# Kernel tuning notes

Hardware: AMD Instinct MI355X
Metric: run time of the kernel (lower is better)

Reference implementation:

```python
import jax, jax.numpy as jnp
import numpy as np

N_NODES = 100000
N_EDGES = 1280000
N_REL = 8
DIM = 64
N_LAYERS = 2
N_TGT = 50000


def setup_inputs() -> dict:
    key = jax.random.key(0)
    ks = jax.random.split(key, 8)
    x_idx = jnp.arange(N_NODES, dtype=jnp.int64) if jax.config.jax_enable_x64 else jnp.arange(N_NODES, dtype=jnp.int32)
    edge_index = jax.random.randint(ks[0], (2, N_EDGES), 0, N_NODES)
    edge_type = jax.random.randint(ks[1], (N_EDGES,), 0, N_REL)
    target_edge_index = jax.random.randint(ks[2], (2, N_TGT), 0, N_NODES)
    # xavier-ish scales to keep activations stable through relu stack
    node_emb = jax.random.normal(ks[3], (N_NODES, DIM), dtype=jnp.float32) * 0.1
    weight = jax.random.normal(ks[4], (N_LAYERS, N_REL, DIM, DIM), dtype=jnp.float32) * (1.0 / np.sqrt(DIM))
    root = jax.random.normal(ks[5], (N_LAYERS, DIM, DIM), dtype=jnp.float32) * (1.0 / np.sqrt(DIM))
    bias = jax.random.normal(ks[6], (N_LAYERS, DIM), dtype=jnp.float32) * 0.01
    return {"x_idx": x_idx, "edge_index": edge_index, "edge_type": edge_type,
            "target_edge_index": target_edge_index, "node_emb": node_emb,
            "weight": weight, "root": root, "bias": bias}


def reference(x_idx, edge_index, edge_type, target_edge_index, node_emb, weight, root, bias):
    # RGCN forward: x = node_emb[x_idx]; L x (FastRGCNConv + relu); edge dot-product score.
    x = node_emb[x_idx]                       # [N, D]
    src, dst = edge_index[0], edge_index[1]   # messages flow src -> dst (PyG source_to_target)
    n = x.shape[0]
    # in-degree for 'mean' aggregation (zero-degree nodes get 0, guard div)
    deg = jax.ops.segment_sum(jnp.ones((src.shape[0],), dtype=x.dtype), dst, num_segments=n)
    inv_deg = (1.0 / jnp.maximum(deg, 1.0))[:, None]  # [N, 1]
    n_layers = weight.shape[0]
    for l in range(n_layers):
        # transform every node by every relation, then gather per edge (FastRGCNConv math)
        h = jnp.einsum('ni,rio->rno', x, weight[l])   # [R, N, D]
        msg = h[edge_type, src]                       # [E, D]
        agg = jax.ops.segment_sum(msg, dst, num_segments=n) * inv_deg  # mean aggr [N, D]
        x = jax.nn.relu(agg + x @ root[l] + bias[l])
    s, t = target_edge_index[0], target_edge_index[1]
    return jnp.sum(x[s] * x[t], axis=-1)              # [T]
```

## Files before the change

### kernel.cpp

```cpp
#include <hip/hip_runtime.h>
#include <hip/hip_bf16.h>

#define DIM 64
#define NREL 8
#define KTOT 576

typedef __bf16 bf16x8 __attribute__((ext_vector_type(8)));
typedef __bf16 bf16x4 __attribute__((ext_vector_type(4)));
typedef float  f32x4  __attribute__((ext_vector_type(4)));

__global__ __launch_bounds__(256) void histgather_kernel(const int* __restrict__ dst,
                                                         const int* __restrict__ et,
                                                         int* __restrict__ deg8,
                                                         int* __restrict__ eoff,
                                                         const int* __restrict__ x_idx,
                                                         const float* __restrict__ emb,
                                                         __bf16* __restrict__ xb0,
                                                         __bf16* __restrict__ hbuf,
                                                         int* __restrict__ srcs,
                                                         int N, int E, int epad_cap) {
    int i = blockIdx.x * 256 + threadIdx.x;
    if (i < N * DIM) {
        int n = i >> 6;
        int c = i & 63;
        xb0[i] = (__bf16)emb[(size_t)x_idx[n] * DIM + c];
    }
    if (i < DIM) {
        hbuf[(size_t)N * NREL * DIM + i] = (__bf16)0.f;
    }
    if (i < epad_cap) srcs[i] = N * NREL;
    if (i < E) eoff[i] = atomicAdd(&deg8[dst[i] * 8 + et[i]], 1);
}

__global__ __launch_bounds__(256) void scan1_kernel(const int* __restrict__ deg8,
                                                    int* __restrict__ offs,
                                                    int* __restrict__ bsum,
                                                    float* __restrict__ invdeg, int N) {
    __shared__ int sd[256];
    int tid = threadIdx.x;
    int d = blockIdx.x * 256 + tid;
    int vpad = 0;
    if (d < N) {
        int vtrue = 0;
#pragma unroll
        for (int r = 0; r < NREL; ++r) vtrue += deg8[d * 8 + r];
        vpad = (vtrue + 3) & ~3;
        invdeg[d] = 1.0f / fmaxf((float)vtrue, 1.0f);
    }
    sd[tid] = vpad;
    __syncthreads();
#pragma unroll
    for (int off = 1; off < 256; off <<= 1) {
        int t = (tid >= off) ? sd[tid - off] : 0;
        __syncthreads();
        sd[tid] += t;
        __syncthreads();
    }
    if (d < N) offs[d] = sd[tid] - vpad;
    if (tid == 255) bsum[blockIdx.x] = sd[255];
}

__global__ __launch_bounds__(512) void scan2wcat_kernel(int* __restrict__ bsum, int nb,
                                                        const float* __restrict__ weight,
                                                        const float* __restrict__ root,
                                                        __bf16* __restrict__ Wt2, int L) {
    if (blockIdx.x == 0) {
        __shared__ int sd[512];
        int tid = threadIdx.x;
        int v = (tid < nb) ? bsum[tid] : 0;
        sd[tid] = v;
        __syncthreads();
#pragma unroll
        for (int off = 1; off < 512; off <<= 1) {
            int t = (tid >= off) ? sd[tid - off] : 0;
            __syncthreads();
            sd[tid] += t;
            __syncthreads();
        }
        if (tid < nb) bsum[tid] = sd[tid] - v;
    } else {
        int idx = (blockIdx.x - 1) * 512 + threadIdx.x;
        int total = L * KTOT * DIM;
        if (idx >= total) return;
        int l = idx / (KTOT * DIM);
        int rem = idx - l * (KTOT * DIM);
        int row = rem / DIM;
        int ch = rem - row * DIM;
        float w;
        if (row < 512) {
            int r = row >> 6, c = row & 63;
            w = weight[(((l * 8 + r) * 64) + ch) * 64 + c];
        } else {
            w = root[(l * 64 + ch) * 64 + (row - 512)];
        }
        Wt2[idx] = (__bf16)w;
    }
}

__global__ __launch_bounds__(256) void rpbuild_kernel(const int* __restrict__ deg8,
                                                      const int* __restrict__ offs,
                                                      const int* __restrict__ bsum,
                                                      int* __restrict__ rp,
                                                      int N) {
    int d = blockIdx.x * 256 + threadIdx.x;
    if (d >= N) return;
    int base = offs[d] + bsum[blockIdx.x];
    int run = 0;
#pragma unroll
    for (int r = 0; r < NREL; ++r) {
        rp[d * 8 + r] = base + run;
        run += deg8[d * 8 + r];
    }
    if (d == N - 1) rp[(size_t)N * 8] = base + ((run + 3) & ~3);
}

__global__ __launch_bounds__(256) void bucket_kernel(const int* __restrict__ src,
                                                     const int* __restrict__ dst,
                                                     const int* __restrict__ et,
                                                     const int* __restrict__ rp,
                                                     const int* __restrict__ eoff,
                                                     int* __restrict__ srcs, int E) {
    int i = blockIdx.x * 256 + threadIdx.x;
    int half = (E + 1) >> 1;
    if (i >= half) return;
    int iB = i + half;
    bool hasB = iB < E;
    int etA = et[i];
    int etB = hasB ? et[iB] : 0;
    int cellA = dst[i] * 8 + etA;
    int cellB = hasB ? dst[iB] * 8 + etB : 0;
    int rA = rp[cellA];
    int rB = hasB ? rp[cellB] : 0;
    int oA = eoff[i];
    int oB = hasB ? eoff[iB] : 0;
    int sA = src[i];
    int sB = hasB ? src[iB] : 0;
    srcs[rA + oA] = sA * NREL + etA;
    if (hasB) srcs[rB + oB] = sB * NREL + etB;
}

__global__ __launch_bounds__(256) void transform_kernel(const __bf16* __restrict__ xin,
                                                        const __bf16* __restrict__ Wt2,
                                                        __bf16* __restrict__ h, int N) {
    int wave = threadIdx.x >> 6;
    int lane = threadIdx.x & 63;
    int l15 = lane & 15;
    int lg  = lane >> 4;

    bf16x8 afrag[8][2];
#pragma unroll
    for (int p = 0; p < 8; ++p) {
        const __bf16* wrow = Wt2 + (size_t)(p * 64 + 16 * wave + l15) * DIM + lg * 8;
        afrag[p][0] = *reinterpret_cast<const bf16x8*>(wrow);
        afrag[p][1] = *reinterpret_cast<const bf16x8*>(wrow + 32);
    }
    int cb = 16 * wave + 4 * lg;

    int ntiles = (N + 15) >> 4;
    for (int tile = blockIdx.x; tile < ntiles; tile += gridDim.x) {
        int n = tile * 16 + l15;
        int nc = (n < N) ? n : (N - 1);
        const __bf16* xrow = xin + (size_t)nc * DIM + lg * 8;
        bf16x8 bv0 = *reinterpret_cast<const bf16x8*>(xrow);
        bf16x8 bv1 = *reinterpret_cast<const bf16x8*>(xrow + 32);

#pragma unroll
        for (int p = 0; p < 8; ++p) {
            f32x4 acc = (f32x4){0.f, 0.f, 0.f, 0.f};
            acc = __builtin_amdgcn_mfma_f32_16x16x32_bf16(afrag[p][0], bv0, acc, 0, 0, 0);
            acc = __builtin_amdgcn_mfma_f32_16x16x32_bf16(afrag[p][1], bv1, acc, 0, 0, 0);
            if (n < N) {
                bf16x4 hv;
#pragma unroll
                for (int i = 0; i < 4; ++i) hv[i] = (__bf16)acc[i];
                *reinterpret_cast<bf16x4*>(h + (size_t)n * (NREL * DIM) + p * 64 + cb) = hv;
            }
        }
    }
}

__global__ __launch_bounds__(256) void aggroot_kernel(const __bf16* __restrict__ h,
                                                      const __bf16* __restrict__ xin,
                                                      const int* __restrict__ srcs,
                                                      const int* __restrict__ rp,
                                                      const float* __restrict__ invdeg,
                                                      const __bf16* __restrict__ Wt2,
                                                      const float* __restrict__ bias_l,
                                                      __bf16* __restrict__ xout, int N) {
    __shared__ __align__(16) float S16[16][68];
    int wave = threadIdx.x >> 6;
    int lane = threadIdx.x & 63;
    int l15 = lane & 15;
    int lg  = lane >> 4;

    bf16x8 ar0, ar1;
    {
        const __bf16* wrow = Wt2 + (size_t)(512 + 16 * wave + l15) * DIM + lg * 8;
        ar0 = *reinterpret_cast<const bf16x8*>(wrow);
        ar1 = *reinterpret_cast<const bf16x8*>(wrow + 32);
    }
    int cbase = 16 * wave + 4 * lg;
    f32x4 bias4 = *reinterpret_cast<const f32x4*>(bias_l + cbase);

    int tile = blockIdx.x;

#pragma unroll
    for (int rr = 0; rr < 4; ++rr) {
        int d0 = tile * 16 + wave * 4 + rr;
        if (d0 >= N) d0 = N - 1;
        int d = __builtin_amdgcn_readfirstlane(d0);
        int qb = rp[d * 8];
        int qe = rp[d * 8 + 8];
        float acc = 0.f;
        int q = qb;
        for (; q + 8 <= qe; q += 8) {
            int4 sa = *reinterpret_cast<const int4*>(srcs + q);
            int4 sb = *reinterpret_cast<const int4*>(srcs + q + 4);
            float v0 = (float)h[(size_t)sa.x * DIM + lane];
            float v1 = (float)h[(size_t)sa.y * DIM + lane];
            float v2 = (float)h[(size_t)sa.z * DIM + lane];
            float v3 = (float)h[(size_t)sa.w * DIM + lane];
            float v4 = (float)h[(size_t)sb.x * DIM + lane];
            float v5 = (float)h[(size_t)sb.y * DIM + lane];
            float v6 = (float)h[(size_t)sb.z * DIM + lane];
            float v7 = (float)h[(size_t)sb.w * DIM + lane];
            acc += ((v0 + v1) + (v2 + v3)) + ((v4 + v5) + (v6 + v7));
        }
        if (q < qe) {
            int4 sa = *reinterpret_cast<const int4*>(srcs + q);
            float v0 = (float)h[(size_t)sa.x * DIM + lane];
            float v1 = (float)h[(size_t)sa.y * DIM + lane];
            float v2 = (float)h[(size_t)sa.z * DIM + lane];
            float v3 = (float)h[(size_t)sa.w * DIM + lane];
            acc += (v0 + v1) + (v2 + v3);
        }
        S16[wave * 4 + rr][lane] = acc * invdeg[d];
    }
    __syncthreads();

    int n = tile * 16 + l15;
    int nc = (n < N) ? n : (N - 1);
    const __bf16* xrow = xin + (size_t)nc * DIM + lg * 8;
    bf16x8 bv0 = *reinterpret_cast<const bf16x8*>(xrow);
    bf16x8 bv1 = *reinterpret_cast<const bf16x8*>(xrow + 32);
    f32x4 acc = (f32x4){0.f, 0.f, 0.f, 0.f};
    acc = __builtin_amdgcn_mfma_f32_16x16x32_bf16(ar0, bv0, acc, 0, 0, 0);
    acc = __builtin_amdgcn_mfma_f32_16x16x32_bf16(ar1, bv1, acc, 0, 0, 0);

    if (n < N) {
        f32x4 ag = *reinterpret_cast<const f32x4*>(&S16[l15][cbase]);
        bf16x4 hv;
#pragma unroll
        for (int i = 0; i < 4; ++i)
            hv[i] = (__bf16)fmaxf(acc[i] + ag[i] + bias4[i], 0.f);
        *reinterpret_cast<bf16x4*>(xout + (size_t)n * DIM + cbase) = hv;
    }
}

__global__ __launch_bounds__(256) void score_kernel(const __bf16* __restrict__ xb,
                                                    const int* __restrict__ s,
                                                    const int* __restrict__ t,
                                                    float* __restrict__ out, int T) {
    int i = blockIdx.x * 4 + (threadIdx.x >> 6);
    if (i >= T) return;
    int lane = threadIdx.x & 63;
    float p = (float)xb[(size_t)s[i] * DIM + lane] * (float)xb[(size_t)t[i] * DIM + lane];
#pragma unroll
    for (int off = 32; off > 0; off >>= 1) p += __shfl_down(p, off, 64);
    if (lane == 0) out[i] = p;
}

extern "C" void kernel_launch(void* const* d_in, const int* in_sizes, int n_in,
                              void* d_out, int out_size, void* d_ws, size_t ws_size,
                              hipStream_t stream) {
    const int*   x_idx  = (const int*)d_in[0];
    const int*   eidx   = (const int*)d_in[1];
    const int*   etyp   = (const int*)d_in[2];
    const int*   tidx   = (const int*)d_in[3];
    const float* emb    = (const float*)d_in[4];
    const float* weight = (const float*)d_in[5];
    const float* root   = (const float*)d_in[6];
    const float* bias   = (const float*)d_in[7];

    int N = in_sizes[0];
    int E = in_sizes[2];
    int T = in_sizes[3] / 2;
    int L = in_sizes[5] / (NREL * DIM * DIM);

    const int* src = eidx;
    const int* dst = eidx + E;
    const int* ts  = tidx;
    const int* tt  = tidx + T;
    float* out = (float*)d_out;

    int epad_cap = E + 3 * N + 64;

    char* p = (char*)d_ws;
    auto alloc = [&](size_t bytes) -> void* {
        void* r = (void*)p;
        p += (bytes + 255) & ~(size_t)255;
        return r;
    };
    __bf16* hbuf    = (__bf16*)alloc(((size_t)N * NREL + 1) * DIM * sizeof(__bf16));
    __bf16* xb0     = (__bf16*)alloc((size_t)N * DIM * sizeof(__bf16));
    __bf16* xb1     = (__bf16*)alloc((size_t)N * DIM * sizeof(__bf16));
    __bf16* Wt2     = (__bf16*)alloc((size_t)L * KTOT * DIM * sizeof(__bf16));
    int*    srcs    = (int*)   alloc((size_t)epad_cap * sizeof(int));
    int*    eoff    = (int*)   alloc((size_t)E * sizeof(int));
    int*    deg8    = (int*)   alloc((size_t)N * 8 * sizeof(int));
    int*    rp      = (int*)   alloc(((size_t)N * 8 + 1) * sizeof(int));
    int*    offs    = (int*)   alloc((size_t)N * sizeof(int));
    float*  invdeg  = (float*) alloc((size_t)N * sizeof(float));
    int*    bsum    = (int*)   alloc(1024 * sizeof(int));

    int nb = (N + 255) / 256;
    int ntiles = (N + 15) / 16;

    hipMemsetAsync(deg8, 0, (size_t)N * 8 * sizeof(int), stream);
    histgather_kernel<<<((size_t)N * DIM + 255) / 256, 256, 0, stream>>>(
        dst, etyp, deg8, eoff, x_idx, emb, xb0, hbuf, srcs, N, E, epad_cap);
    scan1_kernel<<<nb, 256, 0, stream>>>(deg8, offs, bsum, invdeg, N);
    {
        int wtotal = L * KTOT * DIM;
        int wblocks = 1 + (wtotal + 511) / 512;
        scan2wcat_kernel<<<wblocks, 512, 0, stream>>>(bsum, nb, weight, root, Wt2, L);
    }
    rpbuild_kernel<<<nb, 256, 0, stream>>>(deg8, offs, bsum, rp, N);
    {
        int half = (E + 1) / 2;
        bucket_kernel<<<(half + 255) / 256, 256, 0, stream>>>(src, dst, etyp, rp, eoff, srcs, E);
    }

    __bf16* xcur = xb0;
    __bf16* xnxt = xb1;
    for (int l = 0; l < L; ++l) {
        transform_kernel<<<2048, 256, 0, stream>>>(xcur, Wt2 + (size_t)l * KTOT * DIM, hbuf, N);
        aggroot_kernel<<<ntiles, 256, 0, stream>>>(hbuf, xcur, srcs, rp, invdeg,
                                                   Wt2 + (size_t)l * KTOT * DIM,
                                                   bias + (size_t)l * DIM,
                                                   xnxt, N);
        __bf16* tmp = xcur; xcur = xnxt; xnxt = tmp;
    }

    score_kernel<<<(T + 3) / 4, 256, 0, stream>>>(xcur, ts, tt, out, T);
}
```

Before: 367.3 us.

## Fuse layer-0 relation transform into histogram/gather kernel

Moves the layer-0 per-relation transform (x·W_r via MFMA) into the histogram/embedding-gather kernel. The first 2048 blocks do the transform directly from the fp32 embeddings, which removes one separate transform launch and the re-read of xb0. Weight concatenation now runs first as its own kernel, and the block-sum scan is split into a separate single-block kernel. In exchange the histogram kernel carries more register pressure and a grid-stride MFMA loop, and the pipeline gains one extra small launch.

```diff
diff --git a/kernel.cpp b/kernel.cpp
--- a/kernel.cpp
+++ b/kernel.cpp
@@ -4,21 +4,43 @@
 #define DIM 64
 #define NREL 8
 #define KTOT 576
+#define TBLK 2048
 
 typedef __bf16 bf16x8 __attribute__((ext_vector_type(8)));
 typedef __bf16 bf16x4 __attribute__((ext_vector_type(4)));
 typedef float  f32x4  __attribute__((ext_vector_type(4)));
 
-__global__ __launch_bounds__(256) void histgather_kernel(const int* __restrict__ dst,
-                                                         const int* __restrict__ et,
-                                                         int* __restrict__ deg8,
-                                                         int* __restrict__ eoff,
-                                                         const int* __restrict__ x_idx,
-                                                         const float* __restrict__ emb,
-                                                         __bf16* __restrict__ xb0,
-                                                         __bf16* __restrict__ hbuf,
-                                                         int* __restrict__ srcs,
-                                                         int N, int E, int epad_cap) {
+__global__ __launch_bounds__(512) void wcat_kernel(const float* __restrict__ weight,
+                                                   const float* __restrict__ root,
+                                                   __bf16* __restrict__ Wt2, int L) {
+    int idx = blockIdx.x * 512 + threadIdx.x;
+    int total = L * KTOT * DIM;
+    if (idx >= total) return;
+    int l = idx / (KTOT * DIM);
+    int rem = idx - l * (KTOT * DIM);
+    int row = rem / DIM;
+    int ch = rem - row * DIM;
+    float w;
+    if (row < 512) {
+        int r = row >> 6, c = row & 63;
+        w = weight[(((l * 8 + r) * 64) + ch) * 64 + c];
+    } else {
+        w = root[(l * 64 + ch) * 64 + (row - 512)];
+    }
+    Wt2[idx] = (__bf16)w;
+}
+
+__global__ __launch_bounds__(256) void histfused_kernel(const int* __restrict__ dst,
+                                                        const int* __restrict__ et,
+                                                        int* __restrict__ deg8,
+                                                        int* __restrict__ eoff,
+                                                        const int* __restrict__ x_idx,
+                                                        const float* __restrict__ emb,
+                                                        __bf16* __restrict__ xb0,
+                                                        __bf16* __restrict__ hbuf,
+                                                        int* __restrict__ srcs,
+                                                        const __bf16* __restrict__ Wt2,
+                                                        int N, int E, int epad_cap) {
     int i = blockIdx.x * 256 + threadIdx.x;
     if (i < N * DIM) {
         int n = i >> 6;
@@ -30,6 +52,51 @@
     }
     if (i < epad_cap) srcs[i] = N * NREL;
     if (i < E) eoff[i] = atomicAdd(&deg8[dst[i] * 8 + et[i]], 1);
+
+    if (blockIdx.x >= TBLK) return;
+    int wave = threadIdx.x >> 6;
+    int lane = threadIdx.x & 63;
+    int l15 = lane & 15;
+    int lg  = lane >> 4;
+
+    bf16x8 afrag[8][2];
+#pragma unroll
+    for (int p = 0; p < 8; ++p) {
+        const __bf16* wrow = Wt2 + (size_t)(p * 64 + 16 * wave + l15) * DIM + lg * 8;
+        afrag[p][0] = *reinterpret_cast<const bf16x8*>(wrow);
+        afrag[p][1] = *reinterpret_cast<const bf16x8*>(wrow + 32);
+    }
+    int cb = 16 * wave + 4 * lg;
+
+    int ntiles = (N + 15) >> 4;
+    for (int tile = blockIdx.x; tile < ntiles; tile += TBLK) {
+        int n = tile * 16 + l15;
+        int nc = (n < N) ? n : (N - 1);
+        const float* erow = emb + (size_t)x_idx[nc] * DIM + lg * 8;
+        f32x4 e00 = *reinterpret_cast<const f32x4*>(erow);
+        f32x4 e01 = *reinterpret_cast<const f32x4*>(erow + 4);
+        f32x4 e10 = *reinterpret_cast<const f32x4*>(erow + 32);
+        f32x4 e11 = *reinterpret_cast<const f32x4*>(erow + 36);
+        bf16x8 bv0, bv1;
+#pragma unroll
+        for (int j = 0; j < 4; ++j) {
+            bv0[j] = (__bf16)e00[j]; bv0[4 + j] = (__bf16)e01[j];
+            bv1[j] = (__bf16)e10[j]; bv1[4 + j] = (__bf16)e11[j];
+        }
+
+#pragma unroll
+        for (int p = 0; p < 8; ++p) {
+            f32x4 acc = (f32x4){0.f, 0.f, 0.f, 0.f};
+            acc = __builtin_amdgcn_mfma_f32_16x16x32_bf16(afrag[p][0], bv0, acc, 0, 0, 0);
+            acc = __builtin_amdgcn_mfma_f32_16x16x32_bf16(afrag[p][1], bv1, acc, 0, 0, 0);
+            if (n < N) {
+                bf16x4 hv;
+#pragma unroll
+                for (int j = 0; j < 4; ++j) hv[j] = (__bf16)acc[j];
+                *reinterpret_cast<bf16x4*>(hbuf + (size_t)n * (NREL * DIM) + p * 64 + cb) = hv;
+            }
+        }
+    }
 }
 
 __global__ __launch_bounds__(256) void scan1_kernel(const int* __restrict__ deg8,
@@ -60,41 +127,20 @@
     if (tid == 255) bsum[blockIdx.x] = sd[255];
 }
 
-__global__ __launch_bounds__(512) void scan2wcat_kernel(int* __restrict__ bsum, int nb,
-                                                        const float* __restrict__ weight,
-                                                        const float* __restrict__ root,
-                                                        __bf16* __restrict__ Wt2, int L) {
-    if (blockIdx.x == 0) {
-        __shared__ int sd[512];
-        int tid = threadIdx.x;
-        int v = (tid < nb) ? bsum[tid] : 0;
-        sd[tid] = v;
+__global__ __launch_bounds__(512) void bscan_kernel(int* __restrict__ bsum, int nb) {
+    __shared__ int sd[512];
+    int tid = threadIdx.x;
+    int v = (tid < nb) ? bsum[tid] : 0;
+    sd[tid] = v;
+    __syncthreads();
+#pragma unroll
+    for (int off = 1; off < 512; off <<= 1) {
+        int t = (tid >= off) ? sd[tid - off] : 0;
         __syncthreads();
-#pragma unroll
-        for (int off = 1; off < 512; off <<= 1) {
-            int t = (tid >= off) ? sd[tid - off] : 0;
-            __syncthreads();
-            sd[tid] += t;
-            __syncthreads();
-        }
-        if (tid < nb) bsum[tid] = sd[tid] - v;
-    } else {
-        int idx = (blockIdx.x - 1) * 512 + threadIdx.x;
-        int total = L * KTOT * DIM;
-        if (idx >= total) return;
-        int l = idx / (KTOT * DIM);
-        int rem = idx - l * (KTOT * DIM);
-        int row = rem / DIM;
-        int ch = rem - row * DIM;
-        float w;
-        if (row < 512) {
-            int r = row >> 6, c = row & 63;
-            w = weight[(((l * 8 + r) * 64) + ch) * 64 + c];
-        } else {
-            w = root[(l * 64 + ch) * 64 + (row - 512)];
-        }
-        Wt2[idx] = (__bf16)w;
-    }
+        sd[tid] += t;
+        __syncthreads();
+    }
+    if (tid < nb) bsum[tid] = sd[tid] - v;
 }
 
 __global__ __launch_bounds__(256) void rpbuild_kernel(const int* __restrict__ deg8,
@@ -317,14 +363,14 @@
     int ntiles = (N + 15) / 16;
 
     hipMemsetAsync(deg8, 0, (size_t)N * 8 * sizeof(int), stream);
-    histgather_kernel<<<((size_t)N * DIM + 255) / 256, 256, 0, stream>>>(
-        dst, etyp, deg8, eoff, x_idx, emb, xb0, hbuf, srcs, N, E, epad_cap);
-    scan1_kernel<<<nb, 256, 0, stream>>>(deg8, offs, bsum, invdeg, N);
     {
         int wtotal = L * KTOT * DIM;
-        int wblocks = 1 + (wtotal + 511) / 512;
-        scan2wcat_kernel<<<wblocks, 512, 0, stream>>>(bsum, nb, weight, root, Wt2, L);
-    }
+        wcat_kernel<<<(wtotal + 511) / 512, 512, 0, stream>>>(weight, root, Wt2, L);
+    }
+    histfused_kernel<<<((size_t)N * DIM + 255) / 256, 256, 0, stream>>>(
+        dst, etyp, deg8, eoff, x_idx, emb, xb0, hbuf, srcs, Wt2, N, E, epad_cap);
+    scan1_kernel<<<nb, 256, 0, stream>>>(deg8, offs, bsum, invdeg, N);
+    bscan_kernel<<<1, 512, 0, stream>>>(bsum, nb);
     rpbuild_kernel<<<nb, 256, 0, stream>>>(deg8, offs, bsum, rp, N);
     {
         int half = (E + 1) / 2;
@@ -334,7 +380,8 @@
     __bf16* xcur = xb0;
     __bf16* xnxt = xb1;
     for (int l = 0; l < L; ++l) {
-        transform_kernel<<<2048, 256, 0, stream>>>(xcur, Wt2 + (size_t)l * KTOT * DIM, hbuf, N);
+        if (l > 0)
+            transform_kernel<<<2048, 256, 0, stream>>>(xcur, Wt2 + (size_t)l * KTOT * DIM, hbuf, N);
         aggroot_kernel<<<ntiles, 256, 0, stream>>>(hbuf, xcur, srcs, rp, invdeg,
                                                    Wt2 + (size_t)l * KTOT * DIM,
                                                    bias + (size_t)l * DIM,
```

New measurement: 368.6 us. Within noise of the previous version (+0.4%).
